# Kernel optimization log

Measured on AMD Instinct MI355X. Metric: run time of the kernel, lower is better.

## Reference

```python
import jax, jax.numpy as jnp
import numpy as np

B, T, E, A = 512, 64, 1536, 6
STOCH, DETER, HID = 32, 512, 512
MIN_STD = 0.1
EPS = 1e-3  # LayerNorm eps in the torch module


def _ln(x, g, b):
    m = jnp.mean(x, -1, keepdims=True)
    v = jnp.var(x, -1, keepdims=True)
    return (x - m) * jax.lax.rsqrt(v + EPS) * g + b


def setup_inputs() -> dict:
    key = jax.random.key(0)
    ks = jax.random.split(key, 20)
    s = 0.02
    f32 = jnp.float32
    return {
        "embed": jax.random.normal(ks[0], (B, T, E), f32),
        "action": jax.random.normal(ks[1], (B, T, A), f32),
        "reset": jnp.zeros((B, T, 1), f32),
        "noise_post": jax.random.normal(ks[2], (T, B, STOCH), f32),
        "noise_prior": jax.random.normal(ks[3], (T, B, STOCH), f32),
        # params
        "W_inp": jax.random.normal(ks[4], (STOCH + A, HID), f32) * s,
        "g_inp": jnp.ones((HID,), f32),
        "b_inp": jnp.zeros((HID,), f32),
        "W_gru": jax.random.normal(ks[5], (HID + DETER, 3 * DETER), f32) * s,
        "W_img": jax.random.normal(ks[6], (DETER, HID), f32) * s,
        "g_img": jnp.ones((HID,), f32),
        "b_img": jnp.zeros((HID,), f32),
        "W_obs": jax.random.normal(ks[7], (DETER + E, HID), f32) * s,
        "g_obs": jnp.ones((HID,), f32),
        "b_obs": jnp.zeros((HID,), f32),
        "W_ims": jax.random.normal(ks[8], (HID, 2 * STOCH), f32) * s,
        "b_ims": jnp.zeros((2 * STOCH,), f32),
        "W_ostat": jax.random.normal(ks[9], (HID, 2 * STOCH), f32) * s,
        "b_ostat": jnp.zeros((2 * STOCH,), f32),
        "W_init": jax.random.normal(ks[10], (1, DETER), f32) * s,
    }


def reference(embed, action, reset, noise_post, noise_prior,
              W_inp, g_inp, b_inp, W_gru, W_img, g_img, b_img,
              W_obs, g_obs, b_obs, W_ims, b_ims, W_ostat, b_ostat, W_init):
    silu = jax.nn.silu

    def img_out(d):
        return silu(_ln(d @ W_img, g_img, b_img))

    def ims_stats(h):
        st = h @ W_ims + b_ims
        mean, std = jnp.split(st, 2, -1)
        return mean, jax.nn.softplus(std) + MIN_STD

    # initial='learned': deter0 = tanh(W); stoch0 = mode of prior dist = mean
    deter0 = jnp.tanh(W_init) * jnp.ones((B, 1), embed.dtype)  # [B, DETER]
    stoch0, _ = ims_stats(img_out(deter0))                     # [B, STOCH]

    def step(carry, xs):
        stoch, deter = carry
        a, e, r, npost, nprior = xs
        # reset handling: blend prev state with initial state
        a = a * (1.0 - r)
        deter = deter * (1.0 - r) + deter0 * r
        stoch = stoch * (1.0 - r) + stoch0 * r
        # img_step: input MLP
        x = silu(_ln(jnp.concatenate([stoch, a], -1) @ W_inp, g_inp, b_inp))
        # GRUCell (update_bias=-1, tanh cand, no norm)
        parts = jnp.concatenate([x, deter], -1) @ W_gru
        rg, cand, up = jnp.split(parts, 3, -1)
        rg = jax.nn.sigmoid(rg)
        cand = jnp.tanh(rg * cand)
        up = jax.nn.sigmoid(up - 1.0)
        deter_n = up * cand + (1.0 - up) * deter
        # prior stats + reparam sample
        p_mean, p_std = ims_stats(img_out(deter_n))
        p_stoch = p_mean + p_std * nprior
        # posterior (temp_post=True: concat deter with embed)
        h = silu(_ln(jnp.concatenate([deter_n, e], -1) @ W_obs, g_obs, b_obs))
        st = h @ W_ostat + b_ostat
        q_mean, q_std = jnp.split(st, 2, -1)
        q_std = jax.nn.softplus(q_std) + MIN_STD
        q_stoch = q_mean + q_std * npost
        out = jnp.concatenate([q_mean, q_std, q_stoch, p_mean, p_std, p_stoch, deter_n], -1)
        return (q_stoch, deter_n), out

    xs = (jnp.swapaxes(action, 0, 1), jnp.swapaxes(embed, 0, 1),
          jnp.swapaxes(reset, 0, 1), noise_post, noise_prior)
    _, outs = jax.lax.scan(step, (stoch0, deter0), xs)
    # [B, T, 6*STOCH + DETER]
    return jnp.swapaxes(outs, 0, 1)
```

## Files before the change

### kernel.cpp

```cpp
#include <hip/hip_runtime.h>
#include <stdint.h>

typedef unsigned short u16;
typedef unsigned int u32;
typedef __attribute__((ext_vector_type(8))) short bf16x8;
typedef __attribute__((ext_vector_type(4))) float f32x4;

#define DEV __device__ __forceinline__

#define NB 512
#define NT 64
#define NE 1536
#define NH 512
#define NS 32

static constexpr size_t OFF_EOBS   = 0;
static constexpr size_t OFF_XX     = OFF_EOBS + (size_t)NT*NB*512*4;
static constexpr size_t OFF_XD     = OFF_XX + (size_t)512*512*2;
static constexpr size_t OFF_DF     = OFF_XD + (size_t)2*512*512*2;
static constexpr size_t OFF_ACC    = OFF_DF + (size_t)512*512*4;
static constexpr size_t OFF_LNP    = OFF_ACC + (size_t)512*512*4;
static constexpr size_t OFF_D0     = OFF_LNP + (size_t)512*8*2*4;
static constexpr size_t OFF_S0     = OFF_D0 + 512*4;
static constexpr size_t OFF_WINPT  = OFF_S0 + 256;
static constexpr size_t OFF_WGRUT  = OFF_WINPT + (size_t)512*64*2;
static constexpr size_t OFF_WIMGT  = OFF_WGRUT + (size_t)1536*1024*2;
static constexpr size_t OFF_WOBSDT = OFF_WIMGT + (size_t)512*512*2;
static constexpr size_t OFF_WOBSET = OFF_WOBSDT + (size_t)512*512*2;
static constexpr size_t OFF_WIMST  = OFF_WOBSET + (size_t)512*1536*2;
static constexpr size_t OFF_WOSTT  = OFF_WIMST + (size_t)64*512*2;
static constexpr size_t WS_NEED    = OFF_WOSTT + (size_t)64*512*2;

DEV u16 f2b(float f) {
  u32 u = __builtin_bit_cast(u32, f);
  u32 r = (u + 0x7FFFu + ((u >> 16) & 1u)) >> 16;
  return (u16)r;
}
DEV float b2f(u16 h) { u32 u = (u32)h << 16; return __builtin_bit_cast(float, u); }
DEV u32 pk2(float a, float b) { return (u32)f2b(a) | ((u32)f2b(b) << 16); }
DEV float sigf(float x) { return 1.f / (1.f + __expf(-x)); }
DEV float siluf(float x) { return x * sigf(x); }
DEV float softplusf(float x) { return (x > 20.f) ? x : log1pf(__expf(x)); }
DEV f32x4 mfma16(bf16x8 a, bf16x8 b, f32x4 c) {
  return __builtin_amdgcn_mfma_f32_16x16x32_bf16(a, b, c, 0, 0, 0);
}
DEV size_t bswz(int colgrp, int kkmax, int kk, int lane) {
  return (((size_t)colgrp * kkmax + kk) * 64 + lane) * 8;
}

__global__ __launch_bounds__(256) void k_convert(
    const float* __restrict__ W_inp, const float* __restrict__ W_gru,
    const float* __restrict__ W_img, const float* __restrict__ W_obs,
    const float* __restrict__ W_ims, const float* __restrict__ W_ostat,
    char* __restrict__ ws) {
  u16* winpT  = (u16*)(ws + OFF_WINPT);
  u16* wgruT  = (u16*)(ws + OFF_WGRUT);
  u16* wimgT  = (u16*)(ws + OFF_WIMGT);
  u16* wobsdT = (u16*)(ws + OFF_WOBSDT);
  u16* wobseT = (u16*)(ws + OFF_WOBSET);
  u16* wimsT  = (u16*)(ws + OFF_WIMST);
  u16* wostT  = (u16*)(ws + OFF_WOSTT);
  int o = blockIdx.x * 256 + threadIdx.x;
  if (o < 32768) {
    int i = o & 7, lane = (o >> 3) & 63, rem = o >> 9;
    int kk = rem & 1, cg = rem >> 1;
    int col = cg*16 + (lane & 15), k = kk*32 + (lane >> 4)*8 + i;
    winpT[o] = (k < 38) ? f2b(W_inp[k*512 + col]) : (u16)0;
    return;
  }
  o -= 32768;
  if (o < 1572864) {
    int i = o & 7, lane = (o >> 3) & 63, rem = o >> 9;
    int kk = rem & 31, cg = rem >> 5;
    int col = cg*16 + (lane & 15), k = kk*32 + (lane >> 4)*8 + i;
    wgruT[o] = f2b(W_gru[(size_t)k*1536 + col]);
    return;
  }
  o -= 1572864;
  if (o < 262144) {
    int i = o & 7, lane = (o >> 3) & 63, rem = o >> 9;
    int kk = rem & 15, cg = rem >> 4;
    int col = cg*16 + (lane & 15), k = kk*32 + (lane >> 4)*8 + i;
    wimgT[o] = f2b(W_img[k*512 + col]);
    return;
  }
  o -= 262144;
  if (o < 262144) {
    int i = o & 7, lane = (o >> 3) & 63, rem = o >> 9;
    int kk = rem & 15, cg = rem >> 4;
    int col = cg*16 + (lane & 15), k = kk*32 + (lane >> 4)*8 + i;
    wobsdT[o] = f2b(W_obs[k*512 + col]);
    return;
  }
  o -= 262144;
  if (o < 786432) {
    int i = o & 7, lane = (o >> 3) & 63, rem = o >> 9;
    int kk = rem % 48, cg = rem / 48;
    int col = cg*16 + (lane & 15), k = kk*32 + (lane >> 4)*8 + i;
    wobseT[o] = f2b(W_obs[(size_t)(512 + k)*512 + col]);
    return;
  }
  o -= 786432;
  if (o < 32768) {
    int i = o & 7, lane = (o >> 3) & 63, rem = o >> 9;
    int kk = rem & 15, cg = rem >> 4;
    int col = cg*16 + (lane & 15), k = kk*32 + (lane >> 4)*8 + i;
    wimsT[o] = f2b(W_ims[k*64 + col]);
    return;
  }
  o -= 32768;
  {
    int i = o & 7, lane = (o >> 3) & 63, rem = o >> 9;
    int kk = rem & 15, cg = rem >> 4;
    int col = cg*16 + (lane & 15), k = kk*32 + (lane >> 4)*8 + i;
    wostT[o] = f2b(W_ostat[k*64 + col]);
  }
}

__global__ __launch_bounds__(256) void k_init_a(
    const float* __restrict__ W_init, const float* __restrict__ W_img,
    const float* __restrict__ g_img, const float* __restrict__ b_img,
    const float* __restrict__ W_ims, const float* __restrict__ b_ims,
    char* __restrict__ ws) {
  __shared__ float DL[512];
  __shared__ float HL[512];
  __shared__ float RED[256];
  float* d0 = (float*)(ws + OFF_D0);
  float* s0 = (float*)(ws + OFF_S0);
  const int t = threadIdx.x;
  for (int j = t; j < 512; j += 256) { float v = tanhf(W_init[j]); DL[j] = v; d0[j] = v; }
  __syncthreads();
  float pre0 = 0.f, pre1 = 0.f;
  for (int k = 0; k < 512; ++k) {
    float dv = DL[k];
    pre0 += dv * W_img[k*512 + t];
    pre1 += dv * W_img[k*512 + t + 256];
  }
  RED[t] = pre0 + pre1;
  __syncthreads();
  for (int s = 128; s > 0; s >>= 1) { if (t < s) RED[t] += RED[t + s]; __syncthreads(); }
  float m = RED[0] * (1.f/512.f);
  __syncthreads();
  RED[t] = pre0*pre0 + pre1*pre1;
  __syncthreads();
  for (int s = 128; s > 0; s >>= 1) { if (t < s) RED[t] += RED[t + s]; __syncthreads(); }
  float var = RED[0] * (1.f/512.f) - m*m;
  float inv = rsqrtf(var + 1e-3f);
  HL[t]       = siluf((pre0 - m)*inv*g_img[t] + b_img[t]);
  HL[t + 256] = siluf((pre1 - m)*inv*g_img[t+256] + b_img[t+256]);
  __syncthreads();
  if (t < 32) {
    float s = 0.f;
    for (int k = 0; k < 512; ++k) s += HL[k] * W_ims[k*64 + t];
    s0[t] = s + b_ims[t];
  }
}

__global__ __launch_bounds__(256) void k_phase1(
    const float* __restrict__ embed, char* __restrict__ ws) {
  const u16* wobse = (const u16*)(ws + OFF_WOBSET);
  float* eobs = (float*)(ws + OFF_EOBS);
  __shared__ u16 AL[2][32 * 40];
  const int tid = threadIdx.x;
  const int mb = blockIdx.x;
  const int w = tid >> 6, l = tid & 63, l15 = l & 15, lk = l >> 4;
  const f32x4 fz = {0.f, 0.f, 0.f, 0.f};
  f32x4 acc[2][8];
  for (int a = 0; a < 2; ++a) for (int f = 0; f < 8; ++f) acc[a][f] = fz;
  const int srow = tid >> 3, sk4 = (tid & 7) * 4;
  const float* abase = embed + (size_t)(mb*32 + srow)*1536 + sk4;
  const int aoff = srow*40 + sk4;
  {
    float4 v = *(const float4*)(abase);
    uint2 q; q.x = pk2(v.x, v.y); q.y = pk2(v.z, v.w);
    *(uint2*)(AL[0] + aoff) = q;
  }
  float4 vp = *(const float4*)(abase + 32);
  __syncthreads();
  for (int kk = 0; kk < 48; ++kk) {
    if (kk < 47) {
      uint2 q; q.x = pk2(vp.x, vp.y); q.y = pk2(vp.z, vp.w);
      *(uint2*)(AL[(kk+1)&1] + aoff) = q;
    }
    if (kk < 46) vp = *(const float4*)(abase + (kk+2)*32);
    const u16* ALc = AL[kk&1];
    bf16x8 af0 = *(const bf16x8*)(ALc + l15*40 + lk*8);
    bf16x8 af1 = *(const bf16x8*)(ALc + (16 + l15)*40 + lk*8);
    for (int f = 0; f < 8; ++f) {
      bf16x8 bf = *(const bf16x8*)(wobse + bswz(w*8 + f, 48, kk, l));
      acc[0][f] = mfma16(af0, bf, acc[0][f]);
      acc[1][f] = mfma16(af1, bf, acc[1][f]);
    }
    __syncthreads();
  }
  for (int ar = 0; ar < 2; ++ar)
    for (int f = 0; f < 8; ++f) {
      int col = w*128 + f*16 + l15;
      for (int r = 0; r < 4; ++r) {
        int row = mb*32 + ar*16 + lk*4 + r;
        int bb = row >> 6, tt = row & 63;
        __builtin_nontemporal_store(acc[ar][f][r],
            eobs + ((size_t)tt*512 + bb)*512 + col);
      }
    }
}

__global__ __launch_bounds__(512) void k_px0(
    const float* __restrict__ action, const float* __restrict__ reset,
    const float* __restrict__ g_inp, const float* __restrict__ b_inp,
    char* __restrict__ ws) {
  u16* XX = (u16*)(ws + OFF_XX);
  u16* XD0 = (u16*)(ws + OFF_XD);
  float* DF = (float*)(ws + OFF_DF);
  const u16* WINP = (const u16*)(ws + OFF_WINPT);
  const float* d0 = (const float*)(ws + OFF_D0);
  const float* s0 = (const float*)(ws + OFF_S0);
  __shared__ float D0L[512];
  __shared__ float S0L[32];
  __shared__ float STOL[16*32];
  __shared__ float RLC[16];
  __shared__ u16 CIN[16*72];
  __shared__ float LNB[8][16][2];
  const int tid = threadIdx.x;
  const int w = tid >> 6, l = tid & 63, l15 = l & 15, lk = l >> 4;
  const int r0 = blockIdx.x * 16;
  const f32x4 fz = {0.f,0.f,0.f,0.f};
  if (tid < 512) D0L[tid] = d0[tid];
  if (tid < 32) S0L[tid] = s0[tid];
  if (tid < 16) RLC[tid] = reset[(size_t)(r0 + tid)*NT + 0];
  __syncthreads();
  for (int u2 = tid; u2 < 8192; u2 += 512) {
    int rr = u2 >> 9, jj = u2 & 511;
    float v = D0L[jj];
    DF[(size_t)(r0 + rr)*512 + jj] = v;
    XD0[(size_t)(r0 + rr)*512 + jj] = f2b(v);
  }
  if (tid < 512) STOL[tid] = S0L[tid & 31];
  __syncthreads();
  {
    int rr = tid >> 5, kp = (tid & 31)*2;
    float rv = RLC[rr], onem = 1.f - rv;
    int k1 = kp + 1;
    float v0 = (kp < 32) ? (STOL[rr*32+kp]*onem + S0L[kp]*rv)
             : (kp < 38 ? action[((size_t)(r0+rr)*NT + 0)*6 + kp-32]*onem : 0.f);
    float v1 = (k1 < 32) ? (STOL[rr*32+k1]*onem + S0L[k1]*rv)
             : (k1 < 38 ? action[((size_t)(r0+rr)*NT + 0)*6 + k1-32]*onem : 0.f);
    *(u32*)(CIN + rr*72 + kp) = pk2(v0, v1);
  }
  __syncthreads();
  f32x4 ai[4];
  for (int f = 0; f < 4; ++f) ai[f] = fz;
  for (int kk = 0; kk < 2; ++kk) {
    bf16x8 af = *(const bf16x8*)(CIN + l15*72 + kk*32 + lk*8);
    for (int f = 0; f < 4; ++f) {
      bf16x8 bf = *(const bf16x8*)(WINP + bswz(w*4 + f, 2, kk, l));
      ai[f] = mfma16(af, bf, ai[f]);
    }
  }
  for (int r = 0; r < 4; ++r) {
    float s1 = 0.f, s2 = 0.f;
    for (int f = 0; f < 4; ++f) { float v = ai[f][r]; s1 += v; s2 += v*v; }
    for (int d = 1; d < 16; d <<= 1) { s1 += __shfl_xor(s1, d); s2 += __shfl_xor(s2, d); }
    if (l15 == 0) { LNB[w][lk*4 + r][0] = s1; LNB[w][lk*4 + r][1] = s2; }
  }
  __syncthreads();
  float mr[4], ir[4];
  for (int r = 0; r < 4; ++r) {
    int row = lk*4 + r;
    float S1 = 0.f, S2 = 0.f;
    for (int wv = 0; wv < 8; ++wv) { S1 += LNB[wv][row][0]; S2 += LNB[wv][row][1]; }
    float m = S1 * (1.f/512.f);
    float var = S2 * (1.f/512.f) - m*m;
    mr[r] = m; ir[r] = rsqrtf(var + 1e-3f);
  }
  for (int f = 0; f < 4; ++f) {
    int col = w*64 + f*16 + l15;
    float gg = g_inp[col], bb = b_inp[col];
    for (int r = 0; r < 4; ++r)
      XX[(size_t)(r0 + lk*4 + r)*512 + col] = f2b(siluf((ai[f][r] - mr[r]) * ir[r] * gg + bb));
  }
}

__global__ __launch_bounds__(256) void k_gru(
    const float* __restrict__ reset, float* __restrict__ out,
    char* __restrict__ ws, int t) {
  const u16* WGRU = (const u16*)(ws + OFF_WGRUT);
  const u16* XX = (const u16*)(ws + OFF_XX);
  const u16* XDin = (const u16*)(ws + OFF_XD) + (size_t)(t & 1)*512*512;
  u16* XDout = (u16*)(ws + OFF_XD) + (size_t)((t+1) & 1)*512*512;
  float* DF = (float*)(ws + OFF_DF);
  const float* d0 = (const float*)(ws + OFF_D0);
  __shared__ float D0L[512];
  __shared__ float RL[64];
  const int tid = threadIdx.x;
  const int w = tid >> 6, l = tid & 63, l15 = l & 15, lk = l >> 4;
  const int g = blockIdx.x >> 5, p = blockIdx.x & 31;
  const int grow0 = g * 64;
  const int jcol = p*16 + l15;
  const f32x4 fz = {0.f,0.f,0.f,0.f};
  if (tid < 64) RL[tid] = reset[(size_t)(grow0 + tid)*NT + t];
  for (int u2 = tid; u2 < 512; u2 += 256) D0L[u2] = d0[u2];
  __syncthreads();
  const int arow = grow0 + w*16;
  const float rl = RL[w*16 + l15];
  const u16* xrow = XX + (size_t)(arow + l15)*512 + lk*8;
  const u16* drow = XDin + (size_t)(arow + l15)*512 + lk*8;
  f32x4 ag0 = fz, ag1 = fz, ag2 = fz;
  #pragma unroll 4
  for (int kk = 0; kk < 16; ++kk) {
    bf16x8 af = *(const bf16x8*)(xrow + kk*32);
    bf16x8 b0 = *(const bf16x8*)(WGRU + bswz(p,      32, kk, l));
    bf16x8 b1 = *(const bf16x8*)(WGRU + bswz(32 + p, 32, kk, l));
    bf16x8 b2 = *(const bf16x8*)(WGRU + bswz(64 + p, 32, kk, l));
    ag0 = mfma16(af, b0, ag0); ag1 = mfma16(af, b1, ag1); ag2 = mfma16(af, b2, ag2);
  }
  #pragma unroll 4
  for (int kk = 0; kk < 16; ++kk) {
    bf16x8 af = *(const bf16x8*)(drow + kk*32);
    if (rl != 0.f) {
      u16* pp = (u16*)&af;
      for (int i = 0; i < 8; ++i)
        pp[i] = f2b(b2f(pp[i])*(1.f - rl) + D0L[kk*32 + lk*8 + i]*rl);
    }
    bf16x8 b0 = *(const bf16x8*)(WGRU + bswz(p,      32, 16 + kk, l));
    bf16x8 b1 = *(const bf16x8*)(WGRU + bswz(32 + p, 32, 16 + kk, l));
    bf16x8 b2 = *(const bf16x8*)(WGRU + bswz(64 + p, 32, 16 + kk, l));
    ag0 = mfma16(af, b0, ag0); ag1 = mfma16(af, b1, ag1); ag2 = mfma16(af, b2, ag2);
  }
  for (int r = 0; r < 4; ++r) {
    int row = arow + lk*4 + r;
    float rr = RL[w*16 + lk*4 + r];
    size_t idx = (size_t)row*512 + jcol;
    float dold = DF[idx];
    if (rr != 0.f) dold = dold*(1.f - rr) + D0L[jcol]*rr;
    float rg_ = sigf(ag0[r]);
    float ca = tanhf(rg_ * ag1[r]);
    float up = sigf(ag2[r] - 1.f);
    float dn = up*ca + (1.f - up)*dold;
    DF[idx] = dn;
    XDout[idx] = f2b(dn);
    out[((size_t)row*NT + t)*704 + 192 + jcol] = dn;
  }
}

__global__ __launch_bounds__(256) void k_obsA(char* __restrict__ ws, int t) {
  const u16* WOBSD = (const u16*)(ws + OFF_WOBSDT);
  const float* eobs = (const float*)(ws + OFF_EOBS);
  const u16* XDn = (const u16*)(ws + OFF_XD) + (size_t)((t+1) & 1)*512*512;
  float* ACC = (float*)(ws + OFF_ACC);
  float* LNP = (float*)(ws + OFF_LNP);
  __shared__ float LNB[4][16][2];
  const int tid = threadIdx.x;
  const int w = tid >> 6, l = tid & 63, l15 = l & 15, lk = l >> 4;
  const int rg = blockIdx.x >> 3, oc = blockIdx.x & 7;
  const int cg = oc*4 + w;
  const f32x4 fz = {0.f,0.f,0.f,0.f};
  f32x4 ao = fz;
  const u16* abase = XDn + (size_t)(rg*16 + l15)*512 + lk*8;
  #pragma unroll 4
  for (int kk = 0; kk < 16; ++kk) {
    bf16x8 af = *(const bf16x8*)(abase + kk*32);
    bf16x8 bf = *(const bf16x8*)(WOBSD + bswz(cg, 16, kk, l));
    ao = mfma16(af, bf, ao);
  }
  const int col = cg*16 + l15;
  float vs[4];
  for (int r = 0; r < 4; ++r) {
    int row = rg*16 + lk*4 + r;
    float v = ao[r] + eobs[((size_t)t*512 + row)*512 + col];
    vs[r] = v;
    ACC[(size_t)row*512 + col] = v;
  }
  for (int r = 0; r < 4; ++r) {
    float s1 = vs[r], s2 = vs[r]*vs[r];
    for (int d = 1; d < 16; d <<= 1) { s1 += __shfl_xor(s1, d); s2 += __shfl_xor(s2, d); }
    if (l15 == 0) { LNB[w][lk*4 + r][0] = s1; LNB[w][lk*4 + r][1] = s2; }
  }
  __syncthreads();
  if (tid < 16) {
    float S1 = LNB[0][tid][0]+LNB[1][tid][0]+LNB[2][tid][0]+LNB[3][tid][0];
    float S2 = LNB[0][tid][1]+LNB[1][tid][1]+LNB[2][tid][1]+LNB[3][tid][1];
    LNP[((size_t)(rg*16 + tid)*8 + oc)*2]     = S1;
    LNP[((size_t)(rg*16 + tid)*8 + oc)*2 + 1] = S2;
  }
}

__global__ __launch_bounds__(512) void k_obsB(
    const float* __restrict__ action, const float* __restrict__ reset,
    const float* __restrict__ g_inp, const float* __restrict__ b_inp,
    const float* __restrict__ g_obs, const float* __restrict__ b_obs,
    const float* __restrict__ b_ostat, const float* __restrict__ npost,
    float* __restrict__ out, char* __restrict__ ws, int t) {
  const u16* WOST = (const u16*)(ws + OFF_WOSTT);
  const u16* WINP = (const u16*)(ws + OFF_WINPT);
  const float* ACC = (const float*)(ws + OFF_ACC);
  const float* LNP = (const float*)(ws + OFF_LNP);
  u16* XX = (u16*)(ws + OFF_XX);
  const float* s0 = (const float*)(ws + OFF_S0);
  __shared__ u16 HLDS[16*520];
  __shared__ float LNB[8][16][2];
  __shared__ float STL[16*64];
  __shared__ float STOL[16*32];
  __shared__ float RLC[16];
  __shared__ u16 CIN[16*72];
  __shared__ float S0L[32];
  __shared__ float MIV[16][2];
  const int tid = threadIdx.x;
  const int w = tid >> 6, l = tid & 63, l15 = l & 15, lk = l >> 4;
  const int r0 = blockIdx.x * 16;
  const f32x4 fz = {0.f,0.f,0.f,0.f};
  if (tid < 32) S0L[tid] = s0[tid];
  if (tid < 16) {
    float S1 = 0.f, S2 = 0.f;
    for (int o = 0; o < 8; ++o) {
      S1 += LNP[((size_t)(r0 + tid)*8 + o)*2];
      S2 += LNP[((size_t)(r0 + tid)*8 + o)*2 + 1];
    }
    float m = S1 * (1.f/512.f);
    float var = S2 * (1.f/512.f) - m*m;
    MIV[tid][0] = m; MIV[tid][1] = rsqrtf(var + 1e-3f);
  }
  __syncthreads();
  {
    int row = tid >> 5, c0 = (tid & 31)*16;
    float m = MIV[row][0], iv = MIV[row][1];
    const float4* a4 = (const float4*)(ACC + (size_t)(r0+row)*512 + c0);
    const float4* g4 = (const float4*)(g_obs + c0);
    const float4* b4 = (const float4*)(b_obs + c0);
    u16* hrow = HLDS + row*520 + c0;
    for (int q4 = 0; q4 < 4; ++q4) {
      float4 av = a4[q4];
      float4 gv = g4[q4];
      float4 bv = b4[q4];
      float v0 = siluf((av.x - m)*iv*gv.x + bv.x);
      float v1 = siluf((av.y - m)*iv*gv.y + bv.y);
      float v2 = siluf((av.z - m)*iv*gv.z + bv.z);
      float v3 = siluf((av.w - m)*iv*gv.w + bv.w);
      uint2 q; q.x = pk2(v0, v1); q.y = pk2(v2, v3);
      *(uint2*)(hrow + q4*4) = q;
    }
  }
  __syncthreads();
  if (w < 4) {
    f32x4 q = fz;
    #pragma unroll 4
    for (int kk = 0; kk < 16; ++kk) {
      bf16x8 af = *(const bf16x8*)(HLDS + l15*520 + kk*32 + lk*8);
      bf16x8 bf = *(const bf16x8*)(WOST + bswz(w, 16, kk, l));
      q = mfma16(af, bf, q);
    }
    float bia = b_ostat[w*16 + l15];
    for (int r = 0; r < 4; ++r) STL[(lk*4 + r)*64 + w*16 + l15] = q[r] + bia;
  }
  __syncthreads();
  {
    int row = tid >> 5, i = tid & 31;
    float qm = STL[row*64 + i];
    float qs = softplusf(STL[row*64 + 32 + i]) + 0.1f;
    float ns = npost[((size_t)t*512 + r0 + row)*32 + i];
    float qst = qm + qs*ns;
    size_t ob = ((size_t)(r0 + row)*NT + t)*704;
    out[ob + i] = qm;
    out[ob + 32 + i] = qs;
    out[ob + 64 + i] = qst;
    STOL[row*32 + i] = qst;
  }
  __syncthreads();
  if (t < NT - 1) {
    const int tn = t + 1;
    if (tid < 16) RLC[tid] = reset[(size_t)(r0 + tid)*NT + tn];
    __syncthreads();
    {
      int rr = tid >> 5, kp = (tid & 31)*2;
      float rv = RLC[rr], onem = 1.f - rv;
      int k1 = kp + 1;
      float v0 = (kp < 32) ? (STOL[rr*32+kp]*onem + S0L[kp]*rv)
               : (kp < 38 ? action[((size_t)(r0+rr)*NT + tn)*6 + kp-32]*onem : 0.f);
      float v1 = (k1 < 32) ? (STOL[rr*32+k1]*onem + S0L[k1]*rv)
               : (k1 < 38 ? action[((size_t)(r0+rr)*NT + tn)*6 + k1-32]*onem : 0.f);
      *(u32*)(CIN + rr*72 + kp) = pk2(v0, v1);
    }
    __syncthreads();
    f32x4 ai[4];
    for (int f = 0; f < 4; ++f) ai[f] = fz;
    for (int kk = 0; kk < 2; ++kk) {
      bf16x8 af = *(const bf16x8*)(CIN + l15*72 + kk*32 + lk*8);
      for (int f = 0; f < 4; ++f) {
        bf16x8 bf = *(const bf16x8*)(WINP + bswz(w*4 + f, 2, kk, l));
        ai[f] = mfma16(af, bf, ai[f]);
      }
    }
    for (int r = 0; r < 4; ++r) {
      float s1 = 0.f, s2 = 0.f;
      for (int f = 0; f < 4; ++f) { float v = ai[f][r]; s1 += v; s2 += v*v; }
      for (int d = 1; d < 16; d <<= 1) { s1 += __shfl_xor(s1, d); s2 += __shfl_xor(s2, d); }
      if (l15 == 0) { LNB[w][lk*4 + r][0] = s1; LNB[w][lk*4 + r][1] = s2; }
    }
    __syncthreads();
    float mr[4], ir[4];
    for (int r = 0; r < 4; ++r) {
      int row = lk*4 + r;
      float S1 = 0.f, S2 = 0.f;
      for (int wv = 0; wv < 8; ++wv) { S1 += LNB[wv][row][0]; S2 += LNB[wv][row][1]; }
      float m = S1 * (1.f/512.f);
      float var = S2 * (1.f/512.f) - m*m;
      mr[r] = m; ir[r] = rsqrtf(var + 1e-3f);
    }
    for (int f = 0; f < 4; ++f) {
      int col = w*64 + f*16 + l15;
      float gg = g_inp[col], bb = b_inp[col];
      for (int r = 0; r < 4; ++r)
        XX[(size_t)(r0 + lk*4 + r)*512 + col] = f2b(siluf((ai[f][r] - mr[r]) * ir[r] * gg + bb));
    }
  }
}

__global__ __launch_bounds__(256) void k_p3(
    const float* __restrict__ g_img, const float* __restrict__ b_img,
    const float* __restrict__ b_ims, const float* __restrict__ nprior,
    float* __restrict__ out, char* __restrict__ ws) {
  const u16* wimgT = (const u16*)(ws + OFF_WIMGT);
  const u16* wimsT = (const u16*)(ws + OFF_WIMST);
  __shared__ u16 AL[2][32 * 40];
  __shared__ u16 HL[32 * 520];
  __shared__ float LNB[4][32][2];
  __shared__ float STL[32 * 64];
  const int tid = threadIdx.x;
  const int mb = blockIdx.x;
  const int w = tid >> 6, l = tid & 63, l15 = l & 15, lk = l >> 4;
  const f32x4 fz = {0.f,0.f,0.f,0.f};
  f32x4 acc[2][8];
  for (int rb = 0; rb < 2; ++rb) for (int f = 0; f < 8; ++f) acc[rb][f] = fz;
  const int srow = tid >> 3, sko = (tid & 7) * 4;
  const float* sbase = out + (size_t)(mb*32 + srow)*704 + 192 + sko;
  const int aoff = srow*40 + sko;
  {
    float4 v = *(const float4*)(sbase);
    uint2 q; q.x = pk2(v.x, v.y); q.y = pk2(v.z, v.w);
    *(uint2*)(AL[0] + aoff) = q;
  }
  float4 vp = *(const float4*)(sbase + 32);
  __syncthreads();
  for (int kk = 0; kk < 16; ++kk) {
    if (kk < 15) {
      uint2 q; q.x = pk2(vp.x, vp.y); q.y = pk2(vp.z, vp.w);
      *(uint2*)(AL[(kk+1)&1] + aoff) = q;
    }
    if (kk < 14) vp = *(const float4*)(sbase + (kk+2)*32);
    const u16* ALc = AL[kk&1];
    bf16x8 af0 = *(const bf16x8*)(ALc + l15*40 + lk*8);
    bf16x8 af1 = *(const bf16x8*)(ALc + (16 + l15)*40 + lk*8);
    for (int f = 0; f < 8; ++f) {
      bf16x8 bf = *(const bf16x8*)(wimgT + bswz(w*8 + f, 16, kk, l));
      acc[0][f] = mfma16(af0, bf, acc[0][f]);
      acc[1][f] = mfma16(af1, bf, acc[1][f]);
    }
    __syncthreads();
  }
  for (int rb = 0; rb < 2; ++rb) {
    for (int r = 0; r < 4; ++r) {
      float s1 = 0.f, s2 = 0.f;
      for (int f = 0; f < 8; ++f) { float v = acc[rb][f][r]; s1 += v; s2 += v*v; }
      for (int d = 1; d < 16; d <<= 1) { s1 += __shfl_xor(s1, d); s2 += __shfl_xor(s2, d); }
      if (l15 == 0) { LNB[w][rb*16 + lk*4 + r][0] = s1; LNB[w][rb*16 + lk*4 + r][1] = s2; }
    }
  }
  __syncthreads();
  for (int rb = 0; rb < 2; ++rb) {
    float mr[4], ir[4];
    for (int r = 0; r < 4; ++r) {
      int row = rb*16 + lk*4 + r;
      float S1 = LNB[0][row][0] + LNB[1][row][0] + LNB[2][row][0] + LNB[3][row][0];
      float S2 = LNB[0][row][1] + LNB[1][row][1] + LNB[2][row][1] + LNB[3][row][1];
      float m = S1 * (1.f/512.f);
      float var = S2 * (1.f/512.f) - m*m;
      mr[r] = m; ir[r] = rsqrtf(var + 1e-3f);
    }
    for (int f = 0; f < 8; ++f) {
      int col = w*128 + f*16 + l15;
      float gg = g_img[col], bb = b_img[col];
      for (int r = 0; r < 4; ++r) {
        float v = siluf((acc[rb][f][r] - mr[r]) * ir[r] * gg + bb);
        HL[(rb*16 + lk*4 + r)*520 + col] = f2b(v);
      }
    }
  }
  __syncthreads();
  f32x4 q0 = fz, q1 = fz;
  for (int kk = 0; kk < 16; ++kk) {
    bf16x8 bf = *(const bf16x8*)(wimsT + bswz(w, 16, kk, l));
    bf16x8 af0 = *(const bf16x8*)(HL + l15*520 + kk*32 + lk*8);
    bf16x8 af1 = *(const bf16x8*)(HL + (16 + l15)*520 + kk*32 + lk*8);
    q0 = mfma16(af0, bf, q0);
    q1 = mfma16(af1, bf, q1);
  }
  float bia = b_ims[w*16 + l15];
  for (int r = 0; r < 4; ++r) {
    STL[(lk*4 + r)*64 + w*16 + l15] = q0[r] + bia;
    STL[(16 + lk*4 + r)*64 + w*16 + l15] = q1[r] + bia;
  }
  __syncthreads();
  for (int it = tid; it < 1024; it += 256) {
    int row = it >> 5, i = it & 31;
    int grow = mb*32 + row;
    int bb = grow >> 6, tt = grow & 63;
    float pm = STL[row*64 + i];
    float ps = softplusf(STL[row*64 + 32 + i]) + 0.1f;
    float nr = nprior[((size_t)tt*512 + bb)*32 + i];
    float pst = pm + ps*nr;
    size_t ob = (size_t)grow*704;
    out[ob + 96 + i] = pm;
    out[ob + 128 + i] = ps;
    out[ob + 160 + i] = pst;
  }
}

extern "C" void kernel_launch(void* const* d_in, const int* in_sizes, int n_in,
                              void* d_out, int out_size, void* d_ws, size_t ws_size,
                              hipStream_t stream) {
  const float* embed   = (const float*)d_in[0];
  const float* action  = (const float*)d_in[1];
  const float* reset   = (const float*)d_in[2];
  const float* npost   = (const float*)d_in[3];
  const float* nprior  = (const float*)d_in[4];
  const float* W_inp   = (const float*)d_in[5];
  const float* g_inp   = (const float*)d_in[6];
  const float* b_inp   = (const float*)d_in[7];
  const float* W_gru   = (const float*)d_in[8];
  const float* W_img   = (const float*)d_in[9];
  const float* g_img   = (const float*)d_in[10];
  const float* b_img   = (const float*)d_in[11];
  const float* W_obs   = (const float*)d_in[12];
  const float* g_obs   = (const float*)d_in[13];
  const float* b_obs   = (const float*)d_in[14];
  const float* W_ims   = (const float*)d_in[15];
  const float* b_ims   = (const float*)d_in[16];
  const float* W_ostat = (const float*)d_in[17];
  const float* b_ostat = (const float*)d_in[18];
  const float* W_init  = (const float*)d_in[19];
  float* out = (float*)d_out;
  char* ws = (char*)d_ws;
  if (ws_size < WS_NEED) return;

  k_convert<<<11648, 256, 0, stream>>>(W_inp, W_gru, W_img, W_obs, W_ims, W_ostat, ws);
  k_init_a<<<1, 256, 0, stream>>>(W_init, W_img, g_img, b_img, W_ims, b_ims, ws);
  k_phase1<<<1024, 256, 0, stream>>>(embed, ws);
  k_px0<<<32, 512, 0, stream>>>(action, reset, g_inp, b_inp, ws);
  for (int t = 0; t < NT; ++t) {
    k_gru<<<256, 256, 0, stream>>>(reset, out, ws, t);
    k_obsA<<<256, 256, 0, stream>>>(ws, t);
    k_obsB<<<32, 512, 0, stream>>>(action, reset, g_inp, b_inp, g_obs, b_obs,
                                   b_ostat, npost, out, ws, t);
  }
  k_p3<<<1024, 256, 0, stream>>>(g_img, b_img, b_ims, nprior, out, ws);
}
```

Before: 2.269 ms.

## Fuse posterior tail and input projection into GRU kernel, drop per-step obsB launch

Merges the per-step obsB work (posterior LayerNorm/SiLU, ostat projection, sampling, input projection + LN) into the GRU kernel, so each time step takes two launches instead of three and the XX intermediate is kept in LDS. Each of the 256 GRU blocks redundantly recomputes the posterior stats and input projection for its 64 rows (32x redundancy across column blocks), trading extra compute and LDS for fewer launches and global round trips. A tail kernel handles the final step's posterior. The phase1 and p3 loaders also switch from double-buffered LDS prefetch to single-buffer with two barriers per iteration.

New measurement: 4.264 ms. 1.88x slower.

```diff
diff --git a/kernel.cpp b/kernel.cpp
--- a/kernel.cpp
+++ b/kernel.cpp
@@ -160,7 +160,7 @@
     const float* __restrict__ embed, char* __restrict__ ws) {
   const u16* wobse = (const u16*)(ws + OFF_WOBSET);
   float* eobs = (float*)(ws + OFF_EOBS);
-  __shared__ u16 AL[2][32 * 40];
+  __shared__ u16 AL[32 * 40];
   const int tid = threadIdx.x;
   const int mb = blockIdx.x;
   const int w = tid >> 6, l = tid & 63, l15 = l & 15, lk = l >> 4;
@@ -169,29 +169,22 @@
   for (int a = 0; a < 2; ++a) for (int f = 0; f < 8; ++f) acc[a][f] = fz;
   const int srow = tid >> 3, sk4 = (tid & 7) * 4;
   const float* abase = embed + (size_t)(mb*32 + srow)*1536 + sk4;
-  const int aoff = srow*40 + sk4;
-  {
-    float4 v = *(const float4*)(abase);
-    uint2 q; q.x = pk2(v.x, v.y); q.y = pk2(v.z, v.w);
-    *(uint2*)(AL[0] + aoff) = q;
-  }
-  float4 vp = *(const float4*)(abase + 32);
-  __syncthreads();
+  u16* adst = AL + srow*40 + sk4;
   for (int kk = 0; kk < 48; ++kk) {
-    if (kk < 47) {
-      uint2 q; q.x = pk2(vp.x, vp.y); q.y = pk2(vp.z, vp.w);
-      *(uint2*)(AL[(kk+1)&1] + aoff) = q;
-    }
-    if (kk < 46) vp = *(const float4*)(abase + (kk+2)*32);
-    const u16* ALc = AL[kk&1];
-    bf16x8 af0 = *(const bf16x8*)(ALc + l15*40 + lk*8);
-    bf16x8 af1 = *(const bf16x8*)(ALc + (16 + l15)*40 + lk*8);
+    __syncthreads();
+    {
+      float4 v = *(const float4*)(abase + kk*32);
+      uint2 q; q.x = pk2(v.x, v.y); q.y = pk2(v.z, v.w);
+      *(uint2*)adst = q;
+    }
+    __syncthreads();
+    bf16x8 af0 = *(const bf16x8*)(AL + l15*40 + lk*8);
+    bf16x8 af1 = *(const bf16x8*)(AL + (16 + l15)*40 + lk*8);
     for (int f = 0; f < 8; ++f) {
       bf16x8 bf = *(const bf16x8*)(wobse + bswz(w*8 + f, 48, kk, l));
       acc[0][f] = mfma16(af0, bf, acc[0][f]);
       acc[1][f] = mfma16(af1, bf, acc[1][f]);
     }
-    __syncthreads();
   }
   for (int ar = 0; ar < 2; ++ar)
     for (int f = 0; f < 8; ++f) {
@@ -205,141 +198,216 @@
     }
 }
 
-__global__ __launch_bounds__(512) void k_px0(
+__global__ __launch_bounds__(256) void k_gru2(
     const float* __restrict__ action, const float* __restrict__ reset,
     const float* __restrict__ g_inp, const float* __restrict__ b_inp,
-    char* __restrict__ ws) {
-  u16* XX = (u16*)(ws + OFF_XX);
-  u16* XD0 = (u16*)(ws + OFF_XD);
+    const float* __restrict__ g_obs, const float* __restrict__ b_obs,
+    const float* __restrict__ b_ostat, const float* __restrict__ npost,
+    float* __restrict__ out, char* __restrict__ ws, int t) {
+  const u16* WGRU = (const u16*)(ws + OFF_WGRUT);
+  const u16* WOST = (const u16*)(ws + OFF_WOSTT);
+  const u16* WINP = (const u16*)(ws + OFF_WINPT);
+  const float* ACC = (const float*)(ws + OFF_ACC);
+  const float* LNP = (const float*)(ws + OFF_LNP);
+  u16* XD = (u16*)(ws + OFF_XD);
   float* DF = (float*)(ws + OFF_DF);
-  const u16* WINP = (const u16*)(ws + OFF_WINPT);
   const float* d0 = (const float*)(ws + OFF_D0);
   const float* s0 = (const float*)(ws + OFF_S0);
+
+  __shared__ u16 HBUF[64*520];
+  __shared__ u16 CIN[64*72];
+  __shared__ float STL[64*64];
+  __shared__ float STOL[64*32];
+  __shared__ float RLC[64];
   __shared__ float D0L[512];
   __shared__ float S0L[32];
-  __shared__ float STOL[16*32];
-  __shared__ float RLC[16];
-  __shared__ u16 CIN[16*72];
-  __shared__ float LNB[8][16][2];
-  const int tid = threadIdx.x;
-  const int w = tid >> 6, l = tid & 63, l15 = l & 15, lk = l >> 4;
-  const int r0 = blockIdx.x * 16;
-  const f32x4 fz = {0.f,0.f,0.f,0.f};
-  if (tid < 512) D0L[tid] = d0[tid];
-  if (tid < 32) S0L[tid] = s0[tid];
-  if (tid < 16) RLC[tid] = reset[(size_t)(r0 + tid)*NT + 0];
-  __syncthreads();
-  for (int u2 = tid; u2 < 8192; u2 += 512) {
-    int rr = u2 >> 9, jj = u2 & 511;
-    float v = D0L[jj];
-    DF[(size_t)(r0 + rr)*512 + jj] = v;
-    XD0[(size_t)(r0 + rr)*512 + jj] = f2b(v);
-  }
-  if (tid < 512) STOL[tid] = S0L[tid & 31];
-  __syncthreads();
-  {
-    int rr = tid >> 5, kp = (tid & 31)*2;
-    float rv = RLC[rr], onem = 1.f - rv;
-    int k1 = kp + 1;
-    float v0 = (kp < 32) ? (STOL[rr*32+kp]*onem + S0L[kp]*rv)
-             : (kp < 38 ? action[((size_t)(r0+rr)*NT + 0)*6 + kp-32]*onem : 0.f);
-    float v1 = (k1 < 32) ? (STOL[rr*32+k1]*onem + S0L[k1]*rv)
-             : (k1 < 38 ? action[((size_t)(r0+rr)*NT + 0)*6 + k1-32]*onem : 0.f);
-    *(u32*)(CIN + rr*72 + kp) = pk2(v0, v1);
-  }
-  __syncthreads();
-  f32x4 ai[4];
-  for (int f = 0; f < 4; ++f) ai[f] = fz;
-  for (int kk = 0; kk < 2; ++kk) {
-    bf16x8 af = *(const bf16x8*)(CIN + l15*72 + kk*32 + lk*8);
-    for (int f = 0; f < 4; ++f) {
-      bf16x8 bf = *(const bf16x8*)(WINP + bswz(w*4 + f, 2, kk, l));
-      ai[f] = mfma16(af, bf, ai[f]);
-    }
-  }
-  for (int r = 0; r < 4; ++r) {
-    float s1 = 0.f, s2 = 0.f;
-    for (int f = 0; f < 4; ++f) { float v = ai[f][r]; s1 += v; s2 += v*v; }
-    for (int d = 1; d < 16; d <<= 1) { s1 += __shfl_xor(s1, d); s2 += __shfl_xor(s2, d); }
-    if (l15 == 0) { LNB[w][lk*4 + r][0] = s1; LNB[w][lk*4 + r][1] = s2; }
-  }
-  __syncthreads();
-  float mr[4], ir[4];
-  for (int r = 0; r < 4; ++r) {
-    int row = lk*4 + r;
-    float S1 = 0.f, S2 = 0.f;
-    for (int wv = 0; wv < 8; ++wv) { S1 += LNB[wv][row][0]; S2 += LNB[wv][row][1]; }
-    float m = S1 * (1.f/512.f);
-    float var = S2 * (1.f/512.f) - m*m;
-    mr[r] = m; ir[r] = rsqrtf(var + 1e-3f);
-  }
-  for (int f = 0; f < 4; ++f) {
-    int col = w*64 + f*16 + l15;
-    float gg = g_inp[col], bb = b_inp[col];
-    for (int r = 0; r < 4; ++r)
-      XX[(size_t)(r0 + lk*4 + r)*512 + col] = f2b(siluf((ai[f][r] - mr[r]) * ir[r] * gg + bb));
-  }
-}
-
-__global__ __launch_bounds__(256) void k_gru(
-    const float* __restrict__ reset, float* __restrict__ out,
-    char* __restrict__ ws, int t) {
-  const u16* WGRU = (const u16*)(ws + OFF_WGRUT);
-  const u16* XX = (const u16*)(ws + OFF_XX);
-  const u16* XDin = (const u16*)(ws + OFF_XD) + (size_t)(t & 1)*512*512;
-  u16* XDout = (u16*)(ws + OFF_XD) + (size_t)((t+1) & 1)*512*512;
-  float* DF = (float*)(ws + OFF_DF);
-  const float* d0 = (const float*)(ws + OFF_D0);
-  __shared__ float D0L[512];
-  __shared__ float RL[64];
+  __shared__ float MIV[64][2];
+  __shared__ float LNB[4][16][2];
+
   const int tid = threadIdx.x;
   const int w = tid >> 6, l = tid & 63, l15 = l & 15, lk = l >> 4;
   const int g = blockIdx.x >> 5, p = blockIdx.x & 31;
   const int grow0 = g * 64;
   const int jcol = p*16 + l15;
   const f32x4 fz = {0.f,0.f,0.f,0.f};
-  if (tid < 64) RL[tid] = reset[(size_t)(grow0 + tid)*NT + t];
+
   for (int u2 = tid; u2 < 512; u2 += 256) D0L[u2] = d0[u2];
-  __syncthreads();
-  const int arow = grow0 + w*16;
-  const float rl = RL[w*16 + l15];
-  const u16* xrow = XX + (size_t)(arow + l15)*512 + lk*8;
-  const u16* drow = XDin + (size_t)(arow + l15)*512 + lk*8;
-  f32x4 ag0 = fz, ag1 = fz, ag2 = fz;
-  #pragma unroll 4
-  for (int kk = 0; kk < 16; ++kk) {
-    bf16x8 af = *(const bf16x8*)(xrow + kk*32);
-    bf16x8 b0 = *(const bf16x8*)(WGRU + bswz(p,      32, kk, l));
-    bf16x8 b1 = *(const bf16x8*)(WGRU + bswz(32 + p, 32, kk, l));
-    bf16x8 b2 = *(const bf16x8*)(WGRU + bswz(64 + p, 32, kk, l));
-    ag0 = mfma16(af, b0, ag0); ag1 = mfma16(af, b1, ag1); ag2 = mfma16(af, b2, ag2);
-  }
-  #pragma unroll 4
-  for (int kk = 0; kk < 16; ++kk) {
-    bf16x8 af = *(const bf16x8*)(drow + kk*32);
-    if (rl != 0.f) {
-      u16* pp = (u16*)&af;
-      for (int i = 0; i < 8; ++i)
-        pp[i] = f2b(b2f(pp[i])*(1.f - rl) + D0L[kk*32 + lk*8 + i]*rl);
-    }
-    bf16x8 b0 = *(const bf16x8*)(WGRU + bswz(p,      32, 16 + kk, l));
-    bf16x8 b1 = *(const bf16x8*)(WGRU + bswz(32 + p, 32, 16 + kk, l));
-    bf16x8 b2 = *(const bf16x8*)(WGRU + bswz(64 + p, 32, 16 + kk, l));
-    ag0 = mfma16(af, b0, ag0); ag1 = mfma16(af, b1, ag1); ag2 = mfma16(af, b2, ag2);
-  }
-  for (int r = 0; r < 4; ++r) {
-    int row = arow + lk*4 + r;
-    float rr = RL[w*16 + lk*4 + r];
-    size_t idx = (size_t)row*512 + jcol;
-    float dold = DF[idx];
-    if (rr != 0.f) dold = dold*(1.f - rr) + D0L[jcol]*rr;
-    float rg_ = sigf(ag0[r]);
-    float ca = tanhf(rg_ * ag1[r]);
-    float up = sigf(ag2[r] - 1.f);
-    float dn = up*ca + (1.f - up)*dold;
-    DF[idx] = dn;
-    XDout[idx] = f2b(dn);
-    out[((size_t)row*NT + t)*704 + 192 + jcol] = dn;
+  if (tid < 32) S0L[tid] = s0[tid];
+  __syncthreads();
+
+  if (t == 0) {
+    for (int u2 = tid; u2 < 2048; u2 += 256) STOL[u2] = S0L[u2 & 31];
+  } else {
+    const int tm = t - 1;
+    if (tid < 64) {
+      float S1 = 0.f, S2 = 0.f;
+      for (int o = 0; o < 8; ++o) {
+        S1 += LNP[((size_t)(grow0 + tid)*8 + o)*2];
+        S2 += LNP[((size_t)(grow0 + tid)*8 + o)*2 + 1];
+      }
+      float m = S1 * (1.f/512.f);
+      float var = S2 * (1.f/512.f) - m*m;
+      MIV[tid][0] = m; MIV[tid][1] = rsqrtf(var + 1e-3f);
+    }
+    __syncthreads();
+    {
+      int row = tid >> 2, c0 = (tid & 3)*128;
+      float m = MIV[row][0], iv = MIV[row][1];
+      const float4* a4 = (const float4*)(ACC + (size_t)(grow0+row)*512 + c0);
+      const float4* g4 = (const float4*)(g_obs + c0);
+      const float4* b4 = (const float4*)(b_obs + c0);
+      u16* hrow = HBUF + row*520 + c0;
+      for (int q4 = 0; q4 < 32; ++q4) {
+        float4 av = a4[q4];
+        float4 gv = g4[q4];
+        float4 bv = b4[q4];
+        float v0 = siluf((av.x - m)*iv*gv.x + bv.x);
+        float v1 = siluf((av.y - m)*iv*gv.y + bv.y);
+        float v2 = siluf((av.z - m)*iv*gv.z + bv.z);
+        float v3 = siluf((av.w - m)*iv*gv.w + bv.w);
+        uint2 q; q.x = pk2(v0, v1); q.y = pk2(v2, v3);
+        *(uint2*)(hrow + q4*4) = q;
+      }
+    }
+    __syncthreads();
+    {
+      f32x4 q[4];
+      for (int cg = 0; cg < 4; ++cg) q[cg] = fz;
+      #pragma unroll 4
+      for (int kk = 0; kk < 16; ++kk) {
+        bf16x8 af = *(const bf16x8*)(HBUF + (w*16 + l15)*520 + kk*32 + lk*8);
+        for (int cg = 0; cg < 4; ++cg) {
+          bf16x8 bf = *(const bf16x8*)(WOST + bswz(cg, 16, kk, l));
+          q[cg] = mfma16(af, bf, q[cg]);
+        }
+      }
+      for (int cg = 0; cg < 4; ++cg) {
+        float bia = b_ostat[cg*16 + l15];
+        for (int r = 0; r < 4; ++r)
+          STL[(w*16 + lk*4 + r)*64 + cg*16 + l15] = q[cg][r] + bia;
+      }
+    }
+    __syncthreads();
+    for (int u2 = tid; u2 < 2048; u2 += 256) {
+      int row = u2 >> 5, i = u2 & 31;
+      float qm = STL[row*64 + i];
+      float qs = softplusf(STL[row*64 + 32 + i]) + 0.1f;
+      float ns = npost[((size_t)tm*512 + grow0 + row)*32 + i];
+      float qst = qm + qs*ns;
+      STOL[row*32 + i] = qst;
+      if (p == 0) {
+        size_t ob = ((size_t)(grow0 + row)*NT + tm)*704;
+        out[ob + i] = qm;
+        out[ob + 32 + i] = qs;
+        out[ob + 64 + i] = qst;
+      }
+    }
+  }
+  if (tid < 64) RLC[tid] = reset[(size_t)(grow0 + tid)*NT + t];
+  __syncthreads();
+  for (int u2 = tid; u2 < 2048; u2 += 256) {
+    int rr = u2 >> 5, kp = (u2 & 31)*2;
+    float rv = RLC[rr], onem = 1.f - rv;
+    int k1 = kp + 1;
+    float v0 = (kp < 32) ? (STOL[rr*32+kp]*onem + S0L[kp]*rv)
+             : (kp < 38 ? action[((size_t)(grow0+rr)*NT + t)*6 + kp-32]*onem : 0.f);
+    float v1 = (k1 < 32) ? (STOL[rr*32+k1]*onem + S0L[k1]*rv)
+             : (k1 < 38 ? action[((size_t)(grow0+rr)*NT + t)*6 + k1-32]*onem : 0.f);
+    *(u32*)(CIN + rr*72 + kp) = pk2(v0, v1);
+  }
+  __syncthreads();
+  for (int rf = 0; rf < 4; ++rf) {
+    f32x4 ai[8];
+    for (int f = 0; f < 8; ++f) ai[f] = fz;
+    for (int kk = 0; kk < 2; ++kk) {
+      bf16x8 af = *(const bf16x8*)(CIN + (rf*16 + l15)*72 + kk*32 + lk*8);
+      for (int f = 0; f < 8; ++f) {
+        bf16x8 bf = *(const bf16x8*)(WINP + bswz(w*8 + f, 2, kk, l));
+        ai[f] = mfma16(af, bf, ai[f]);
+      }
+    }
+    for (int r = 0; r < 4; ++r) {
+      float s1 = 0.f, s2 = 0.f;
+      for (int f = 0; f < 8; ++f) { float v = ai[f][r]; s1 += v; s2 += v*v; }
+      for (int d = 1; d < 16; d <<= 1) { s1 += __shfl_xor(s1, d); s2 += __shfl_xor(s2, d); }
+      if (l15 == 0) { LNB[w][lk*4 + r][0] = s1; LNB[w][lk*4 + r][1] = s2; }
+    }
+    __syncthreads();
+    float mr[4], ir[4];
+    for (int r = 0; r < 4; ++r) {
+      int row = lk*4 + r;
+      float S1 = LNB[0][row][0]+LNB[1][row][0]+LNB[2][row][0]+LNB[3][row][0];
+      float S2 = LNB[0][row][1]+LNB[1][row][1]+LNB[2][row][1]+LNB[3][row][1];
+      float m = S1 * (1.f/512.f);
+      float var = S2 * (1.f/512.f) - m*m;
+      mr[r] = m; ir[r] = rsqrtf(var + 1e-3f);
+    }
+    for (int f = 0; f < 8; ++f) {
+      int col = w*128 + f*16 + l15;
+      float gg = g_inp[col], bb = b_inp[col];
+      for (int r = 0; r < 4; ++r)
+        HBUF[(rf*16 + lk*4 + r)*520 + col] = f2b(siluf((ai[f][r] - mr[r]) * ir[r] * gg + bb));
+    }
+    __syncthreads();
+  }
+  {
+    const u16* XDin = (const u16*)XD + (size_t)(t & 1)*512*512;
+    u16* XDout = XD + (size_t)((t+1) & 1)*512*512;
+    const int arow = grow0 + w*16;
+    const float rl = RLC[w*16 + l15];
+    f32x4 ag0 = fz, ag1 = fz, ag2 = fz;
+    #pragma unroll 4
+    for (int kk = 0; kk < 16; ++kk) {
+      bf16x8 af = *(const bf16x8*)(HBUF + (w*16 + l15)*520 + kk*32 + lk*8);
+      bf16x8 b0 = *(const bf16x8*)(WGRU + bswz(p,      32, kk, l));
+      bf16x8 b1 = *(const bf16x8*)(WGRU + bswz(32 + p, 32, kk, l));
+      bf16x8 b2 = *(const bf16x8*)(WGRU + bswz(64 + p, 32, kk, l));
+      ag0 = mfma16(af, b0, ag0); ag1 = mfma16(af, b1, ag1); ag2 = mfma16(af, b2, ag2);
+    }
+    if (t == 0) {
+      #pragma unroll 4
+      for (int kk = 0; kk < 16; ++kk) {
+        union { u16 h[8]; bf16x8 v; } u;
+        for (int i = 0; i < 8; ++i) u.h[i] = f2b(D0L[kk*32 + lk*8 + i]);
+        bf16x8 b0 = *(const bf16x8*)(WGRU + bswz(p,      32, 16 + kk, l));
+        bf16x8 b1 = *(const bf16x8*)(WGRU + bswz(32 + p, 32, 16 + kk, l));
+        bf16x8 b2 = *(const bf16x8*)(WGRU + bswz(64 + p, 32, 16 + kk, l));
+        ag0 = mfma16(u.v, b0, ag0); ag1 = mfma16(u.v, b1, ag1); ag2 = mfma16(u.v, b2, ag2);
+      }
+    } else {
+      const u16* drow = XDin + (size_t)(arow + l15)*512 + lk*8;
+      #pragma unroll 4
+      for (int kk = 0; kk < 16; ++kk) {
+        bf16x8 af = *(const bf16x8*)(drow + kk*32);
+        if (rl != 0.f) {
+          u16* pp = (u16*)&af;
+          for (int i = 0; i < 8; ++i)
+            pp[i] = f2b(b2f(pp[i])*(1.f - rl) + D0L[kk*32 + lk*8 + i]*rl);
+        }
+        bf16x8 b0 = *(const bf16x8*)(WGRU + bswz(p,      32, 16 + kk, l));
+        bf16x8 b1 = *(const bf16x8*)(WGRU + bswz(32 + p, 32, 16 + kk, l));
+        bf16x8 b2 = *(const bf16x8*)(WGRU + bswz(64 + p, 32, 16 + kk, l));
+        ag0 = mfma16(af, b0, ag0); ag1 = mfma16(af, b1, ag1); ag2 = mfma16(af, b2, ag2);
+      }
+    }
+    for (int r = 0; r < 4; ++r) {
+      int row = arow + lk*4 + r;
+      float rr = RLC[w*16 + lk*4 + r];
+      size_t idx = (size_t)row*512 + jcol;
+      float dold;
+      if (t == 0) dold = D0L[jcol];
+      else {
+        dold = DF[idx];
+        if (rr != 0.f) dold = dold*(1.f - rr) + D0L[jcol]*rr;
+      }
+      float rg_ = sigf(ag0[r]);
+      float ca = tanhf(rg_ * ag1[r]);
+      float up = sigf(ag2[r] - 1.f);
+      float dn = up*ca + (1.f - up)*dold;
+      DF[idx] = dn;
+      XDout[idx] = f2b(dn);
+      out[((size_t)row*NT + t)*704 + 192 + jcol] = dn;
+    }
   }
 }
 
@@ -385,31 +453,21 @@
   }
 }
 
-__global__ __launch_bounds__(512) void k_obsB(
-    const float* __restrict__ action, const float* __restrict__ reset,
-    const float* __restrict__ g_inp, const float* __restrict__ b_inp,
+__global__ __launch_bounds__(512) void k_tail(
     const float* __restrict__ g_obs, const float* __restrict__ b_obs,
     const float* __restrict__ b_ostat, const float* __restrict__ npost,
-    float* __restrict__ out, char* __restrict__ ws, int t) {
+    float* __restrict__ out, char* __restrict__ ws) {
   const u16* WOST = (const u16*)(ws + OFF_WOSTT);
-  const u16* WINP = (const u16*)(ws + OFF_WINPT);
   const float* ACC = (const float*)(ws + OFF_ACC);
   const float* LNP = (const float*)(ws + OFF_LNP);
-  u16* XX = (u16*)(ws + OFF_XX);
-  const float* s0 = (const float*)(ws + OFF_S0);
   __shared__ u16 HLDS[16*520];
-  __shared__ float LNB[8][16][2];
   __shared__ float STL[16*64];
-  __shared__ float STOL[16*32];
-  __shared__ float RLC[16];
-  __shared__ u16 CIN[16*72];
-  __shared__ float S0L[32];
   __shared__ float MIV[16][2];
   const int tid = threadIdx.x;
   const int w = tid >> 6, l = tid & 63, l15 = l & 15, lk = l >> 4;
   const int r0 = blockIdx.x * 16;
+  const int t = NT - 1;
   const f32x4 fz = {0.f,0.f,0.f,0.f};
-  if (tid < 32) S0L[tid] = s0[tid];
   if (tid < 16) {
     float S1 = 0.f, S2 = 0.f;
     for (int o = 0; o < 8; ++o) {
@@ -463,55 +521,6 @@
     out[ob + i] = qm;
     out[ob + 32 + i] = qs;
     out[ob + 64 + i] = qst;
-    STOL[row*32 + i] = qst;
-  }
-  __syncthreads();
-  if (t < NT - 1) {
-    const int tn = t + 1;
-    if (tid < 16) RLC[tid] = reset[(size_t)(r0 + tid)*NT + tn];
-    __syncthreads();
-    {
-      int rr = tid >> 5, kp = (tid & 31)*2;
-      float rv = RLC[rr], onem = 1.f - rv;
-      int k1 = kp + 1;
-      float v0 = (kp < 32) ? (STOL[rr*32+kp]*onem + S0L[kp]*rv)
-               : (kp < 38 ? action[((size_t)(r0+rr)*NT + tn)*6 + kp-32]*onem : 0.f);
-      float v1 = (k1 < 32) ? (STOL[rr*32+k1]*onem + S0L[k1]*rv)
-               : (k1 < 38 ? action[((size_t)(r0+rr)*NT + tn)*6 + k1-32]*onem : 0.f);
-      *(u32*)(CIN + rr*72 + kp) = pk2(v0, v1);
-    }
-    __syncthreads();
-    f32x4 ai[4];
-    for (int f = 0; f < 4; ++f) ai[f] = fz;
-    for (int kk = 0; kk < 2; ++kk) {
-      bf16x8 af = *(const bf16x8*)(CIN + l15*72 + kk*32 + lk*8);
-      for (int f = 0; f < 4; ++f) {
-        bf16x8 bf = *(const bf16x8*)(WINP + bswz(w*4 + f, 2, kk, l));
-        ai[f] = mfma16(af, bf, ai[f]);
-      }
-    }
-    for (int r = 0; r < 4; ++r) {
-      float s1 = 0.f, s2 = 0.f;
-      for (int f = 0; f < 4; ++f) { float v = ai[f][r]; s1 += v; s2 += v*v; }
-      for (int d = 1; d < 16; d <<= 1) { s1 += __shfl_xor(s1, d); s2 += __shfl_xor(s2, d); }
-      if (l15 == 0) { LNB[w][lk*4 + r][0] = s1; LNB[w][lk*4 + r][1] = s2; }
-    }
-    __syncthreads();
-    float mr[4], ir[4];
-    for (int r = 0; r < 4; ++r) {
-      int row = lk*4 + r;
-      float S1 = 0.f, S2 = 0.f;
-      for (int wv = 0; wv < 8; ++wv) { S1 += LNB[wv][row][0]; S2 += LNB[wv][row][1]; }
-      float m = S1 * (1.f/512.f);
-      float var = S2 * (1.f/512.f) - m*m;
-      mr[r] = m; ir[r] = rsqrtf(var + 1e-3f);
-    }
-    for (int f = 0; f < 4; ++f) {
-      int col = w*64 + f*16 + l15;
-      float gg = g_inp[col], bb = b_inp[col];
-      for (int r = 0; r < 4; ++r)
-        XX[(size_t)(r0 + lk*4 + r)*512 + col] = f2b(siluf((ai[f][r] - mr[r]) * ir[r] * gg + bb));
-    }
   }
 }
 
@@ -521,7 +530,7 @@
     float* __restrict__ out, char* __restrict__ ws) {
   const u16* wimgT = (const u16*)(ws + OFF_WIMGT);
   const u16* wimsT = (const u16*)(ws + OFF_WIMST);
-  __shared__ u16 AL[2][32 * 40];
+  __shared__ u16 AL[32 * 40];
   __shared__ u16 HL[32 * 520];
   __shared__ float LNB[4][32][2];
   __shared__ float STL[32 * 64];
@@ -533,29 +542,22 @@
   for (int rb = 0; rb < 2; ++rb) for (int f = 0; f < 8; ++f) acc[rb][f] = fz;
   const int srow = tid >> 3, sko = (tid & 7) * 4;
   const float* sbase = out + (size_t)(mb*32 + srow)*704 + 192 + sko;
-  const int aoff = srow*40 + sko;
-  {
-    float4 v = *(const float4*)(sbase);
-    uint2 q; q.x = pk2(v.x, v.y); q.y = pk2(v.z, v.w);
-    *(uint2*)(AL[0] + aoff) = q;
-  }
-  float4 vp = *(const float4*)(sbase + 32);
-  __syncthreads();
+  u16* sdst = AL + srow*40 + sko;
   for (int kk = 0; kk < 16; ++kk) {
-    if (kk < 15) {
-      uint2 q; q.x = pk2(vp.x, vp.y); q.y = pk2(vp.z, vp.w);
-      *(uint2*)(AL[(kk+1)&1] + aoff) = q;
-    }
-    if (kk < 14) vp = *(const float4*)(sbase + (kk+2)*32);
-    const u16* ALc = AL[kk&1];
-    bf16x8 af0 = *(const bf16x8*)(ALc + l15*40 + lk*8);
-    bf16x8 af1 = *(const bf16x8*)(ALc + (16 + l15)*40 + lk*8);
+    __syncthreads();
+    {
+      float4 v = *(const float4*)(sbase + kk*32);
+      uint2 q; q.x = pk2(v.x, v.y); q.y = pk2(v.z, v.w);
+      *(uint2*)sdst = q;
+    }
+    __syncthreads();
+    bf16x8 af0 = *(const bf16x8*)(AL + l15*40 + lk*8);
+    bf16x8 af1 = *(const bf16x8*)(AL + (16 + l15)*40 + lk*8);
     for (int f = 0; f < 8; ++f) {
       bf16x8 bf = *(const bf16x8*)(wimgT + bswz(w*8 + f, 16, kk, l));
       acc[0][f] = mfma16(af0, bf, acc[0][f]);
       acc[1][f] = mfma16(af1, bf, acc[1][f]);
     }
-    __syncthreads();
   }
   for (int rb = 0; rb < 2; ++rb) {
     for (int r = 0; r < 4; ++r) {
@@ -645,12 +647,11 @@
   k_convert<<<11648, 256, 0, stream>>>(W_inp, W_gru, W_img, W_obs, W_ims, W_ostat, ws);
   k_init_a<<<1, 256, 0, stream>>>(W_init, W_img, g_img, b_img, W_ims, b_ims, ws);
   k_phase1<<<1024, 256, 0, stream>>>(embed, ws);
-  k_px0<<<32, 512, 0, stream>>>(action, reset, g_inp, b_inp, ws);
   for (int t = 0; t < NT; ++t) {
-    k_gru<<<256, 256, 0, stream>>>(reset, out, ws, t);
+    k_gru2<<<256, 256, 0, stream>>>(action, reset, g_inp, b_inp, g_obs, b_obs,
+                                    b_ostat, npost, out, ws, t);
     k_obsA<<<256, 256, 0, stream>>>(ws, t);
-    k_obsB<<<32, 512, 0, stream>>>(action, reset, g_inp, b_inp, g_obs, b_obs,
-                                   b_ostat, npost, out, ws, t);
-  }
+  }
+  k_tail<<<32, 512, 0, stream>>>(g_obs, b_obs, b_ostat, npost, out, ws);
   k_p3<<<1024, 256, 0, stream>>>(g_img, b_img, b_ims, nprior, out, ws);
 }
```
